# Performance work log

Measured on AMD Instinct MI355X. Metric: run time of the kernel, lower is better.

## Reference

```python
import jax, jax.numpy as jnp
import numpy as np

THRESH = 1.0
BETA = 0.9
SG_ALPHA = 2.0  # snntorch ATan surrogate default alpha

@jax.custom_vjp
def spike(u):
    # Heaviside fire: 1 where membrane exceeds threshold
    return (u > 0).astype(u.dtype)

def _spike_fwd(u):
    return spike(u), u

def _spike_bwd(u, g):
    # snntorch ATan surrogate gradient: (alpha/2) / (1 + (pi/2*alpha*u)^2)
    return (g * (SG_ALPHA / 2) / (1.0 + (jnp.pi / 2 * SG_ALPHA * u) ** 2),)

spike.defvjp(_spike_fwd, _spike_bwd)

def setup_inputs() -> dict:
    key = jax.random.key(0)
    k1, k2, k3 = jax.random.split(key, 3)
    T, B, N_IN, N1, N2 = 64, 256, 2048, 1024, 1024
    # Bernoulli(0.2) binary input spike trains
    input_spikes = (jax.random.uniform(k1, (T, B, N_IN)) < 0.2).astype(jnp.float32)
    s = 1.0 / np.sqrt(N_IN)  # nn.Linear default init range
    W1 = jax.random.uniform(k2, (N1, N_IN), minval=-s, maxval=s, dtype=jnp.float32)
    W2 = jax.random.uniform(k3, (N2, N_IN), minval=-s, maxval=s, dtype=jnp.float32)
    return {"input_spikes": input_spikes, "W1": W1, "W2": W2}

def _lif_layer(cur_seq, beta, thr):
    # cur_seq: [T, B, N] post-synaptic currents. snntorch Leaky, reset-by-subtraction:
    #   reset_t = H(mem_{t-1} - thr); mem_t = beta*mem_{t-1} + cur_t - reset_t*thr; spk_t = H(mem_t - thr)
    def step(mem, cur):
        reset = spike(mem - thr)
        mem = beta * mem + cur - reset * thr
        spk = spike(mem - thr)
        return mem, (spk, mem)
    init_mem = jnp.zeros_like(cur_seq[0])
    _, (spk_rec, mem_rec) = jax.lax.scan(step, init_mem, cur_seq)
    return spk_rec, mem_rec  # each [T, B, N]

def reference(input_spikes, W1, W2):
    # Source quirk (faithful): every fc layer consumes the raw input spikes.
    cur1 = jnp.einsum('tbi,ni->tbn', input_spikes, W1)  # [T,B,N1]
    cur2 = jnp.einsum('tbi,ni->tbn', input_spikes, W2)  # [T,B,N2]
    spk1, mem1 = _lif_layer(cur1, BETA, THRESH)
    spk2, mem2 = _lif_layer(cur2, BETA, THRESH)
    return spk1, mem1, spk2, mem2
```

## Files before the change

### kernel.cpp

```cpp
#include <hip/hip_runtime.h>
#include <hip/hip_bf16.h>
#include <stdint.h>


#define REGION 16777216
#define BN_ELEMS 262144
#define FLAG_EPS 3e-4f

typedef __attribute__((ext_vector_type(4))) int v4i;

typedef __attribute__((address_space(1))) const void gvoid_t;
typedef __attribute__((address_space(3))) void svoid_t;

__device__ __forceinline__ void gload_lds16(const void* g, void* l) {
  __builtin_amdgcn_global_load_lds((gvoid_t*)g, (svoid_t*)l, 16, 0, 0);
}

__global__ void cvt_mask(const float* __restrict__ spikes, int* __restrict__ s4,
                         unsigned long long* __restrict__ maskR) {
  int id = blockIdx.x * 256 + threadIdx.x;
  int row = id >> 5, c = id & 31;
  const float4* p = (const float4*)(spikes + (long long)row * 2048 + c * 64);
  unsigned long long m = 0;
  int* sd = s4 + (row * 2048 + c * 64) / 4;
#pragma unroll
  for (int q = 0; q < 16; ++q) {
    float4 v = p[q];
    int b0 = (v.x != 0.f), b1 = (v.y != 0.f), b2 = (v.z != 0.f), b3 = (v.w != 0.f);
    sd[q] = b0 | (b1 << 8) | (b2 << 16) | (b3 << 24);
    m |= (unsigned long long)b0 << (4 * q);
    m |= (unsigned long long)b1 << (4 * q + 1);
    m |= (unsigned long long)b2 << (4 * q + 2);
    m |= (unsigned long long)b3 << (4 * q + 3);
  }
  maskR[(long long)row * 32 + c] = m;
}

__global__ void pack_digits(const float* __restrict__ W1, const float* __restrict__ W2,
                            signed char* __restrict__ Bp) {
  int idx = blockIdx.x * 256 + threadIdx.x;
  if (idx >= 2048 * 2048) return;
  int n = idx >> 11, k = idx & 2047;
  float w = (n < 1024) ? W1[n * 2048 + k] : W2[(n - 1024) * 2048 + k];
  int V = (int)rintf(w * 1048576.0f);
  int d0 = ((V + 128) & 255) - 128;
  int d1 = (V - d0) >> 8;
  signed char* row = Bp + (long long)n * 4096;
  row[k]        = (signed char)d1;
  row[2048 + k] = (signed char)d0;
}

__global__ __launch_bounds__(512) void gemm_snn(const signed char* __restrict__ S,
                                                const signed char* __restrict__ Bp,
                                                float* __restrict__ out) {
  __shared__ __align__(16) signed char As[2][8192];
  __shared__ __align__(16) signed char Bs0[2][8192];
  __shared__ __align__(16) signed char Bs1[2][8192];
  const int tid = threadIdx.x;
  const int wv = tid >> 6, ln = tid & 63;

  int bid = blockIdx.x;
  int swz = (bid & 7) * 128 + (bid >> 3);
  const int bm = swz >> 3;
  const int bn = swz & 7;
  const int wr = wv >> 2, wc = wv & 3;

  const int srow = wv * 16 + (ln >> 2);
  const int scolb = ((ln & 3) ^ ((srow >> 1) & 3)) * 16;
  const signed char* aSrc  = S  + (long long)(bm * 128 + srow) * 2048 + scolb;
  const signed char* b0Src = Bp + (long long)(bn * 128 + srow) * 4096 + scolb;
  const signed char* b1Src = Bp + (long long)(1024 + bn * 128 + srow) * 4096 + scolb;
  const int ldsW = wv * 1024;

  const int l15 = ln & 15, l4 = ln >> 4;
  int aOff[4], bOff[2];
#pragma unroll
  for (int f = 0; f < 4; ++f) {
    int r = wr * 64 + f * 16 + l15;
    aOff[f] = r * 64 + (l4 ^ ((r >> 1) & 3)) * 16;
  }
#pragma unroll
  for (int g = 0; g < 2; ++g) {
    int r = wc * 32 + g * 16 + l15;
    bOff[g] = r * 64 + (l4 ^ ((r >> 1) & 3)) * 16;
  }

  v4i acc[2][4][2];
#pragma unroll
  for (int L = 0; L < 2; ++L)
#pragma unroll
    for (int f = 0; f < 4; ++f)
#pragma unroll
      for (int g = 0; g < 2; ++g) acc[L][f][g] = (v4i){0, 0, 0, 0};

  gload_lds16(aSrc, &As[0][ldsW]);
  gload_lds16(b0Src, &Bs0[0][ldsW]);
  gload_lds16(b1Src, &Bs1[0][ldsW]);

#pragma unroll 1
  for (int i = 0; i < 64; ++i) {
    const int p = i & 1;
    if (i < 63) {
      const int ii = i + 1;
      const int kc = (ii & 31) * 64, so = (ii >> 5) * 2048;
      gload_lds16(aSrc + kc, &As[p ^ 1][ldsW]);
      gload_lds16(b0Src + so + kc, &Bs0[p ^ 1][ldsW]);
      gload_lds16(b1Src + so + kc, &Bs1[p ^ 1][ldsW]);
      asm volatile("s_waitcnt vmcnt(3)" ::: "memory");
    } else {
      asm volatile("s_waitcnt vmcnt(0)" ::: "memory");
    }
    __builtin_amdgcn_sched_barrier(0);
    __builtin_amdgcn_s_barrier();
    __builtin_amdgcn_sched_barrier(0);

    if (i == 32) {
#pragma unroll
      for (int L = 0; L < 2; ++L)
#pragma unroll
        for (int f = 0; f < 4; ++f)
#pragma unroll
          for (int g = 0; g < 2; ++g)
#pragma unroll
            for (int r = 0; r < 4; ++r) acc[L][f][g][r] *= 256;
    }

    v4i a[4], b0[2], b1[2];
#pragma unroll
    for (int f = 0; f < 4; ++f) a[f] = *(const v4i*)&As[p][aOff[f]];
#pragma unroll
    for (int g = 0; g < 2; ++g) b0[g] = *(const v4i*)&Bs0[p][bOff[g]];
#pragma unroll
    for (int g = 0; g < 2; ++g) b1[g] = *(const v4i*)&Bs1[p][bOff[g]];
#pragma unroll
    for (int f = 0; f < 4; ++f)
#pragma unroll
      for (int g = 0; g < 2; ++g) {
        acc[0][f][g] = __builtin_amdgcn_mfma_i32_16x16x64_i8(a[f], b0[g], acc[0][f][g], 0, 0, 0);
        acc[1][f][g] = __builtin_amdgcn_mfma_i32_16x16x64_i8(a[f], b1[g], acc[1][f][g], 0, 0, 0);
      }
    __builtin_amdgcn_sched_barrier(0);
    __builtin_amdgcn_s_barrier();
    __builtin_amdgcn_sched_barrier(0);
  }

#pragma unroll
  for (int L = 0; L < 2; ++L) {
    float* spkBase = out + (L ? 2LL * REGION : 0);
#pragma unroll
    for (int f = 0; f < 4; ++f)
#pragma unroll
      for (int g = 0; g < 2; ++g) {
        int row = bm * 128 + wr * 64 + f * 16 + l4 * 4;
        int col = bn * 128 + wc * 32 + g * 16 + l15;
#pragma unroll
        for (int r = 0; r < 4; ++r)
          spkBase[(long long)(row + r) * 1024 + col] =
              (float)((double)acc[L][f][g][r] * (1.0 / 1048576.0));
      }
  }
}

__global__ void zero_count(int* count) { if (threadIdx.x == 0) *count = 0; }

__global__ void lif_flag(float* __restrict__ out, int* __restrict__ list,
                         int* __restrict__ count) {
  int idx = blockIdx.x * 256 + threadIdx.x;
  int layer = idx >> 18;
  int j = idx & (BN_ELEMS - 1);
  float* spk = out + (layer ? 2LL * REGION : 0);
  float* mem = out + (layer ? 3LL * REGION : 1LL * REGION);
  float m = 0.0f;
  bool flag = false;
#pragma unroll 1
  for (int t = 0; t < 64; ++t) {
    int k = t * BN_ELEMS + j;
    float c = spk[k];
    float reset = (m > 1.0f) ? 1.0f : 0.0f;
    m = __fsub_rn(__fadd_rn(__fmul_rn(0.9f, m), c), reset);
    flag |= (fabsf(m - 1.0f) < FLAG_EPS);
    spk[k] = (m > 1.0f) ? 1.0f : 0.0f;
    mem[k] = m;
  }
  if (flag) { int p = atomicAdd(count, 1); list[p] = idx; }
}

__global__ __launch_bounds__(256) void fixup_kernel(
    const unsigned long long* __restrict__ maskR,
    const float* __restrict__ W1, const float* __restrict__ W2,
    const int* __restrict__ list, const int* __restrict__ count,
    float* __restrict__ out) {
  __shared__ float ws[4][2048];
  __shared__ float curs[4][64];
  const int wv = threadIdx.x >> 6, ln = threadIdx.x & 63;
  const int cnt = *count;
  for (int li = blockIdx.x * 4 + wv; li < cnt; li += gridDim.x * 4) {
    int idx = list[li];
    int layer = idx >> 18;
    int j = idx & (BN_ELEMS - 1);
    int n = j & 1023, b = j >> 10;
    const float* wrow = (layer ? W2 : W1) + (long long)n * 2048;
#pragma unroll
    for (int i = 0; i < 8; ++i)
      ((float4*)ws[wv])[ln + 64 * i] = ((const float4*)wrow)[ln + 64 * i];
    asm volatile("s_waitcnt lgkmcnt(0)" ::: "memory");

    const unsigned long long* mr = maskR + (long long)(ln * 256 + b) * 32;
    float total = 0.0f, pacc = 0.0f;
    bool first = true;
#pragma unroll 1
    for (int c = 0; c < 32; ++c) {
      if (c == 6 || c == 12 || c == 18 || c == 24 || c == 30) {
        total = first ? pacc : __fadd_rn(total, pacc);
        first = false; pacc = 0.0f;
      }
      unsigned long long msk = mr[c];
      unsigned mlo = (unsigned)msk, mhi = (unsigned)(msk >> 32);
      const float* wb = ws[wv] + c * 64;
      while (mlo) {
        int q = __builtin_ctz(mlo);
        mlo &= mlo - 1;
        pacc = __fadd_rn(pacc, wb[q]);
      }
      while (mhi) {
        int q = __builtin_ctz(mhi);
        mhi &= mhi - 1;
        pacc = __fadd_rn(pacc, wb[32 + q]);
      }
    }
    total = first ? pacc : __fadd_rn(total, pacc);
    curs[wv][ln] = total;
    asm volatile("s_waitcnt lgkmcnt(0)" ::: "memory");

    float m = 0.0f, myspk = 0.0f, mymem = 0.0f;
#pragma unroll 1
    for (int tt = 0; tt < 64; ++tt) {
      float c2 = curs[wv][tt];
      float reset = (m > 1.0f) ? 1.0f : 0.0f;
      m = __fsub_rn(__fadd_rn(__fmul_rn(0.9f, m), c2), reset);
      if (tt == ln) { myspk = (m > 1.0f) ? 1.0f : 0.0f; mymem = m; }
    }
    float* spkR = out + (layer ? 2LL * REGION : 0);
    float* memR = out + (layer ? 3LL * REGION : 1LL * REGION);
    spkR[ln * BN_ELEMS + j] = myspk;
    memR[ln * BN_ELEMS + j] = mymem;
  }
}

extern "C" void kernel_launch(void* const* d_in, const int* in_sizes, int n_in,
                              void* d_out, int out_size, void* d_ws, size_t ws_size,
                              hipStream_t stream) {
  const float* spikes = (const float*)d_in[0];
  const float* W1 = (const float*)d_in[1];
  const float* W2 = (const float*)d_in[2];
  float* out = (float*)d_out;
  signed char* Bp = (signed char*)d_ws;
  signed char* S  = (signed char*)d_ws + 8388608;
  unsigned long long* maskR = (unsigned long long*)((char*)d_ws + 41943040);
  int* list  = (int*)((char*)d_ws + 46137344);
  int* count = (int*)((char*)d_ws + 48234496);

  cvt_mask<<<2048, 256, 0, stream>>>(spikes, (int*)S, maskR);
  pack_digits<<<16384, 256, 0, stream>>>(W1, W2, Bp);
  gemm_snn<<<1024, 512, 0, stream>>>(S, Bp, out);
  zero_count<<<1, 64, 0, stream>>>(count);
  lif_flag<<<2048, 256, 0, stream>>>(out, list, count);
  fixup_kernel<<<4096, 256, 0, stream>>>(maskR, W1, W2, list, count, out);
}
```

Measured before the change: 350.2 us.

## Triple-buffer GEMM LDS to drop second barrier, fuse counter reset, dual-layer LIF

The GEMM mainloop moves from double to triple LDS buffering. This lets it drop the trailing per-iteration barrier, since a buffer being read can no longer be overwritten by the next prefetch. The separate zero_count launch is folded into cvt_mask. lif_flag now processes both layers per thread with half the blocks, which exposes more independent loads per thread. The costs are higher LDS use (72KB per block), which may reduce occupancy, and a possible race on the count reset if it is not ordered before later kernels, though stream ordering covers it.

```diff
diff --git a/kernel.cpp b/kernel.cpp
--- a/kernel.cpp
+++ b/kernel.cpp
@@ -17,8 +17,10 @@
 }
 
 __global__ void cvt_mask(const float* __restrict__ spikes, int* __restrict__ s4,
-                         unsigned long long* __restrict__ maskR) {
+                         unsigned long long* __restrict__ maskR,
+                         int* __restrict__ count) {
   int id = blockIdx.x * 256 + threadIdx.x;
+  if (id == 0) *count = 0;
   int row = id >> 5, c = id & 31;
   const float4* p = (const float4*)(spikes + (long long)row * 2048 + c * 64);
   unsigned long long m = 0;
@@ -53,9 +55,9 @@
 __global__ __launch_bounds__(512) void gemm_snn(const signed char* __restrict__ S,
                                                 const signed char* __restrict__ Bp,
                                                 float* __restrict__ out) {
-  __shared__ __align__(16) signed char As[2][8192];
-  __shared__ __align__(16) signed char Bs0[2][8192];
-  __shared__ __align__(16) signed char Bs1[2][8192];
+  __shared__ __align__(16) signed char As[3 * 8192];
+  __shared__ __align__(16) signed char Bs0[3 * 8192];
+  __shared__ __align__(16) signed char Bs1[3 * 8192];
   const int tid = threadIdx.x;
   const int wv = tid >> 6, ln = tid & 63;
 
@@ -93,19 +95,20 @@
 #pragma unroll
       for (int g = 0; g < 2; ++g) acc[L][f][g] = (v4i){0, 0, 0, 0};
 
-  gload_lds16(aSrc, &As[0][ldsW]);
-  gload_lds16(b0Src, &Bs0[0][ldsW]);
-  gload_lds16(b1Src, &Bs1[0][ldsW]);
-
+  gload_lds16(aSrc, &As[ldsW]);
+  gload_lds16(b0Src, &Bs0[ldsW]);
+  gload_lds16(b1Src, &Bs1[ldsW]);
+
+  int p = 0, pn = 1;
 #pragma unroll 1
   for (int i = 0; i < 64; ++i) {
-    const int p = i & 1;
     if (i < 63) {
       const int ii = i + 1;
       const int kc = (ii & 31) * 64, so = (ii >> 5) * 2048;
-      gload_lds16(aSrc + kc, &As[p ^ 1][ldsW]);
-      gload_lds16(b0Src + so + kc, &Bs0[p ^ 1][ldsW]);
-      gload_lds16(b1Src + so + kc, &Bs1[p ^ 1][ldsW]);
+      const int wb = pn * 8192 + ldsW;
+      gload_lds16(aSrc + kc, &As[wb]);
+      gload_lds16(b0Src + so + kc, &Bs0[wb]);
+      gload_lds16(b1Src + so + kc, &Bs1[wb]);
       asm volatile("s_waitcnt vmcnt(3)" ::: "memory");
     } else {
       asm volatile("s_waitcnt vmcnt(0)" ::: "memory");
@@ -125,13 +128,14 @@
             for (int r = 0; r < 4; ++r) acc[L][f][g][r] *= 256;
     }
 
+    const int rb = p * 8192;
     v4i a[4], b0[2], b1[2];
 #pragma unroll
-    for (int f = 0; f < 4; ++f) a[f] = *(const v4i*)&As[p][aOff[f]];
-#pragma unroll
-    for (int g = 0; g < 2; ++g) b0[g] = *(const v4i*)&Bs0[p][bOff[g]];
-#pragma unroll
-    for (int g = 0; g < 2; ++g) b1[g] = *(const v4i*)&Bs1[p][bOff[g]];
+    for (int f = 0; f < 4; ++f) a[f] = *(const v4i*)&As[rb + aOff[f]];
+#pragma unroll
+    for (int g = 0; g < 2; ++g) b0[g] = *(const v4i*)&Bs0[rb + bOff[g]];
+#pragma unroll
+    for (int g = 0; g < 2; ++g) b1[g] = *(const v4i*)&Bs1[rb + bOff[g]];
 #pragma unroll
     for (int f = 0; f < 4; ++f)
 #pragma unroll
@@ -139,9 +143,7 @@
         acc[0][f][g] = __builtin_amdgcn_mfma_i32_16x16x64_i8(a[f], b0[g], acc[0][f][g], 0, 0, 0);
         acc[1][f][g] = __builtin_amdgcn_mfma_i32_16x16x64_i8(a[f], b1[g], acc[1][f][g], 0, 0, 0);
       }
-    __builtin_amdgcn_sched_barrier(0);
-    __builtin_amdgcn_s_barrier();
-    __builtin_amdgcn_sched_barrier(0);
+    p = pn; pn = (pn == 2) ? 0 : pn + 1;
   }
 
 #pragma unroll
@@ -161,28 +163,33 @@
   }
 }
 
-__global__ void zero_count(int* count) { if (threadIdx.x == 0) *count = 0; }
-
 __global__ void lif_flag(float* __restrict__ out, int* __restrict__ list,
                          int* __restrict__ count) {
-  int idx = blockIdx.x * 256 + threadIdx.x;
-  int layer = idx >> 18;
-  int j = idx & (BN_ELEMS - 1);
-  float* spk = out + (layer ? 2LL * REGION : 0);
-  float* mem = out + (layer ? 3LL * REGION : 1LL * REGION);
-  float m = 0.0f;
-  bool flag = false;
+  int j = blockIdx.x * 256 + threadIdx.x;
+  float* spk1 = out;
+  float* mem1 = out + 1LL * REGION;
+  float* spk2 = out + 2LL * REGION;
+  float* mem2 = out + 3LL * REGION;
+  float ma = 0.0f, mb = 0.0f;
+  bool fa = false, fb = false;
 #pragma unroll 1
   for (int t = 0; t < 64; ++t) {
     int k = t * BN_ELEMS + j;
-    float c = spk[k];
-    float reset = (m > 1.0f) ? 1.0f : 0.0f;
-    m = __fsub_rn(__fadd_rn(__fmul_rn(0.9f, m), c), reset);
-    flag |= (fabsf(m - 1.0f) < FLAG_EPS);
-    spk[k] = (m > 1.0f) ? 1.0f : 0.0f;
-    mem[k] = m;
-  }
-  if (flag) { int p = atomicAdd(count, 1); list[p] = idx; }
+    float ca = spk1[k];
+    float cb = spk2[k];
+    float ra = (ma > 1.0f) ? 1.0f : 0.0f;
+    float rb = (mb > 1.0f) ? 1.0f : 0.0f;
+    ma = __fsub_rn(__fadd_rn(__fmul_rn(0.9f, ma), ca), ra);
+    mb = __fsub_rn(__fadd_rn(__fmul_rn(0.9f, mb), cb), rb);
+    fa |= (fabsf(ma - 1.0f) < FLAG_EPS);
+    fb |= (fabsf(mb - 1.0f) < FLAG_EPS);
+    spk1[k] = (ma > 1.0f) ? 1.0f : 0.0f;
+    mem1[k] = ma;
+    spk2[k] = (mb > 1.0f) ? 1.0f : 0.0f;
+    mem2[k] = mb;
+  }
+  if (fa) { int q = atomicAdd(count, 1); list[q] = j; }
+  if (fb) { int q = atomicAdd(count, 1); list[q] = BN_ELEMS + j; }
 }
 
 __global__ __launch_bounds__(256) void fixup_kernel(
@@ -260,10 +267,9 @@
   int* list  = (int*)((char*)d_ws + 46137344);
   int* count = (int*)((char*)d_ws + 48234496);
 
-  cvt_mask<<<2048, 256, 0, stream>>>(spikes, (int*)S, maskR);
+  cvt_mask<<<2048, 256, 0, stream>>>(spikes, (int*)S, maskR, count);
   pack_digits<<<16384, 256, 0, stream>>>(W1, W2, Bp);
   gemm_snn<<<1024, 512, 0, stream>>>(S, Bp, out);
-  zero_count<<<1, 64, 0, stream>>>(count);
-  lif_flag<<<2048, 256, 0, stream>>>(out, list, count);
+  lif_flag<<<1024, 256, 0, stream>>>(out, list, count);
   fixup_kernel<<<4096, 256, 0, stream>>>(maskR, W1, W2, list, count, out);
 }
```

Measured after the change: 343.0 us. -2.0%, faster.
